# Performance work log

Hardware: AMD Instinct MI355X
Metric: run time of the kernel (lower is better)

The kernel has to match this reference:

```python
import jax, jax.numpy as jnp
import numpy as np
from jax import lax

BETA_CONTENT = 1.0   # content_addressing default beta
BETA_TOPK = 10.0     # top_k_attention default beta
GAMMA = 1.5          # location sharpening
ERASE = 0.5          # erase_strength for write
EPS = 1e-8
NEG = -1.0e9

N_SLOTS, SLOT_D, BATCH, K = 65536, 256, 512, 64


def _l2norm(x):
    # F.normalize: x / max(||x||, 1e-12)
    n = jnp.sqrt(jnp.sum(x * x, axis=-1, keepdims=True))
    return x / jnp.maximum(n, 1e-12)


def setup_inputs() -> dict:
    key = jax.random.key(0)
    k1, k2, k3, k4, k5 = jax.random.split(key, 5)
    return {
        "memory": jax.random.normal(k1, (N_SLOTS, SLOT_D), dtype=jnp.float32) * 0.1,
        "query": jax.random.normal(k2, (BATCH, SLOT_D), dtype=jnp.float32),
        "value": jax.random.normal(k3, (BATCH, SLOT_D), dtype=jnp.float32),
        "prev_weights": jax.random.uniform(k4, (BATCH, N_SLOTS), dtype=jnp.float32),
        "shift_weights": jax.random.uniform(k5, (3,), dtype=jnp.float32),
        "k": K,
    }


def reference(memory, query, value, prev_weights, shift_weights, k):
    B, N = query.shape[0], memory.shape[0]
    # --- content addressing: cosine sim + softmax ---
    qn = _l2norm(query)                      # [B,D]
    mn = _l2norm(memory)                     # [N,D]
    sim = qn @ mn.T                          # [B,N]
    w_content = jax.nn.softmax(BETA_CONTENT * sim, axis=-1)
    read_content = w_content @ memory        # [B,D] read via content weights

    # --- top-k attention: soft threshold mask + softmax ---
    kk = min(int(k), N)
    topk_vals, _ = lax.top_k(sim, kk)        # [B,kk]
    thr = topk_vals[:, -1:]                  # kth largest similarity
    mask = jax.nn.sigmoid(BETA_TOPK * (sim - thr))
    w_topk = jax.nn.softmax(BETA_TOPK * sim + (1.0 - mask) * NEG, axis=-1)
    read_topk = w_topk @ memory              # [B,D]

    # --- location addressing: conv1d shift (padding=1) + gamma sharpen ---
    p = jnp.pad(prev_weights, ((0, 0), (1, 1)))  # [B,N+2]
    shifted = (p[:, :-2] * shift_weights[0]
               + p[:, 1:-1] * shift_weights[1]
               + p[:, 2:] * shift_weights[2])     # [B,N]
    sharp = shifted ** GAMMA
    w_loc = sharp / (jnp.sum(sharp, axis=-1, keepdims=True) + EPS)

    # --- write: softmax(address), multiplicative erase, additive write ---
    w_write = jax.nn.softmax(w_loc, axis=-1)          # write() softmaxes its input
    erase_factor = jnp.prod(1.0 - w_write * ERASE, axis=0)   # [N] sequential erases fused
    new_mem = memory * erase_factor[:, None] + w_write.T @ value  # [N,D]

    return jnp.concatenate([read_content.reshape(-1),
                            read_topk.reshape(-1),
                            new_mem.reshape(-1)])
```

## Files before the change

kernel.cpp:

```cpp
#include <hip/hip_runtime.h>
#include <math.h>

#define BATCH   512
#define NSLOTS  65536
#define DIM     256

#define RB      64
#define NROWG   (BATCH/RB)
#define NCG     64
#define CPG     (NSLOTS/NCG)
#define ST      32
#define NTILES  (CPG/ST)
#define DELTA   0.009f

#define WS_QN   0
#define WS_RN   (WS_QN + BATCH*DIM)
#define WS_WST  (WS_RN + NSLOTS)
#define WS_DEN  (WS_WST + BATCH*4)
#define WS_ZS   (WS_DEN + BATCH)
#define WS_ZZ   (WS_ZS + BATCH)
#define WS_SST  (WS_ZZ + BATCH)
#define WS_VT   (WS_SST + BATCH*NCG*16*4)
#define WS_MN   (WS_VT + (BATCH*DIM)/2)
#define WS_MT   (WS_MN + ((size_t)NSLOTS*DIM)/2)

typedef __attribute__((ext_vector_type(8))) short bf16x8;
typedef __attribute__((ext_vector_type(4))) float f32x4;

__device__ inline unsigned short f2b(float x){
  unsigned u = __float_as_uint(x);
  unsigned r = u + 0x7FFFu + ((u >> 16) & 1u);
  return (unsigned short)(r >> 16);
}
__device__ inline float b2f(unsigned short b){
  return __uint_as_float(((unsigned)b) << 16);
}

__device__ __forceinline__ void gl16(const void* g, void* l){
  __builtin_amdgcn_global_load_lds(
      (__attribute__((address_space(1))) void*)g,
      (__attribute__((address_space(3))) void*)l, 16, 0, 0);
}

#define SBAR_LGKM() do{ asm volatile("s_waitcnt lgkmcnt(0)" ::: "memory"); \
                        __builtin_amdgcn_s_barrier();                      \
                        asm volatile("" ::: "memory"); }while(0)
#define SBAR_ALL()  do{ asm volatile("s_waitcnt vmcnt(0) lgkmcnt(0)" ::: "memory"); \
                        __builtin_amdgcn_s_barrier();                               \
                        asm volatile("" ::: "memory"); }while(0)

__global__ __launch_bounds__(256) void k_qnorm(const float* __restrict__ q, float* __restrict__ qn){
  int b = blockIdx.x, t = threadIdx.x;
  float v = q[b*DIM + t];
  __shared__ float red[256];
  red[t] = v*v;
  __syncthreads();
  for (int s = 128; s > 0; s >>= 1){
    if (t < s) red[t] += red[t+s];
    __syncthreads();
  }
  float n = fmaxf(sqrtf(red[0]), 1e-12f);
  qn[b*DIM + t] = v / n;
}

__global__ __launch_bounds__(256) void k_mnprep(const float* __restrict__ mem,
                                                float* __restrict__ rn,
                                                unsigned short* __restrict__ MN){
  __shared__ float rns[64];
  int t = threadIdx.x;
  int s0 = blockIdx.x * 64;
  int w = t >> 6, ln = t & 63;
  #pragma unroll
  for (int it = 0; it < 16; ++it){
    int r = it*4 + w;
    float4 v = ((const float4*)(mem + (size_t)(s0 + r)*DIM))[ln];
    float s = v.x*v.x + v.y*v.y + v.z*v.z + v.w*v.w;
    #pragma unroll
    for (int off = 32; off > 0; off >>= 1) s += __shfl_xor(s, off, 64);
    if (ln == 0){
      float inv = 1.0f / fmaxf(sqrtf(s), 1e-12f);
      rns[r] = inv; rn[s0 + r] = inv;
    }
  }
  __syncthreads();
  #pragma unroll
  for (int j = 0; j < 8; ++j){
    int id = j*256 + t;
    int r = id >> 5;
    int c = id & 31;
    float inv = rns[r];
    const float4* p = (const float4*)(mem + (size_t)(s0 + r)*DIM + c*8);
    float4 a = p[0], b = p[1];
    bf16x8 o;
    o[0]=(short)f2b(a.x*inv); o[1]=(short)f2b(a.y*inv); o[2]=(short)f2b(a.z*inv); o[3]=(short)f2b(a.w*inv);
    o[4]=(short)f2b(b.x*inv); o[5]=(short)f2b(b.y*inv); o[6]=(short)f2b(b.z*inv); o[7]=(short)f2b(b.w*inv);
    *(bf16x8*)&MN[(size_t)(s0 + r)*DIM + ((c ^ (r & 7))*8)] = o;
  }
}

__global__ __launch_bounds__(256) void k_mtprep(const float* __restrict__ mem, unsigned short* __restrict__ MT){
  __shared__ __align__(16) unsigned short tile[64][68];
  int sb = (blockIdx.x >> 2)*64, dd = (blockIdx.x & 3)*64;
  int t = threadIdx.x;
  int w = t >> 6, ln = t & 63;
  #pragma unroll
  for (int k = 0; k < 4; ++k){
    int sl = w*16 + k*4 + (ln >> 4);
    int doff = (ln & 15)*4;
    float4 f = *(const float4*)&mem[(size_t)(sb + sl)*DIM + dd + doff];
    tile[doff+0][sl] = f2b(f.x);
    tile[doff+1][sl] = f2b(f.y);
    tile[doff+2][sl] = f2b(f.z);
    tile[doff+3][sl] = f2b(f.w);
  }
  __syncthreads();
  #pragma unroll
  for (int k = 0; k < 4; ++k){
    int dl = w*16 + k*4 + (ln >> 4);
    int boff = (ln & 15)*4;
    int B = boff >> 5;
    int p = (boff >> 3) & 3;
    int pp = p ^ ((dl >> 1) & 3);
    int off = B*32 + pp*8 + (boff & 7);
    *(short4*)&MT[(size_t)(dd + dl)*NSLOTS + sb + off] = *(const short4*)&tile[dl][boff];
  }
}

__global__ __launch_bounds__(256) void k_prep(const float* __restrict__ val, unsigned short* __restrict__ VT){
  __shared__ __align__(16) unsigned short tile[64][68];
  int bb = (blockIdx.x >> 2)*64, dd = (blockIdx.x & 3)*64;
  int t = threadIdx.x;
  int w = t >> 6, ln = t & 63;
  #pragma unroll
  for (int k = 0; k < 4; ++k){
    int bl = w*16 + k*4 + (ln >> 4);
    int doff = (ln & 15)*4;
    float4 f = *(const float4*)&val[(size_t)(bb + bl)*DIM + dd + doff];
    tile[doff+0][bl] = f2b(f.x);
    tile[doff+1][bl] = f2b(f.y);
    tile[doff+2][bl] = f2b(f.z);
    tile[doff+3][bl] = f2b(f.w);
  }
  __syncthreads();
  #pragma unroll
  for (int k = 0; k < 4; ++k){
    int dl = w*16 + k*4 + (ln >> 4);
    int boff = (ln & 15)*4;
    int c  = (bb + boff) >> 5;
    int p  = (boff >> 3) & 3;
    int pp = p ^ ((dl >> 1) & 3);
    size_t addr = (size_t)c*8192 + (size_t)(dd + dl)*32 + pp*8 + (boff & 7);
    *(short4*)&VT[addr] = *(const short4*)&tile[dl][boff];
  }
}

__global__ __launch_bounds__(256) void k_ws1(const float* __restrict__ prev, const float* __restrict__ sw,
                                             float* __restrict__ zs){
  int blk = blockIdx.x;
  int b = blk >> 4, ch = blk & 15;
  int t = threadIdx.x;
  int w = t >> 6, lane = t & 63;
  float s0 = sw[0], s1 = sw[1], s2 = sw[2];
  const float* p = prev + (size_t)b*NSLOTS;
  const float4* p4 = (const float4*)p;
  float lsum = 0.f;
  #pragma unroll
  for (int k = 0; k < 4; ++k){
    int i4 = ch*1024 + k*256 + t;
    float4 f = p4[i4];
    float lft = (i4 > 0) ? p[4*i4 - 1] : 0.f;
    float rgt = (i4 < NSLOTS/4 - 1) ? p[4*i4 + 4] : 0.f;
    float sh0 = s0*lft + s1*f.x + s2*f.y;
    float sh1 = s0*f.x + s1*f.y + s2*f.z;
    float sh2 = s0*f.y + s1*f.z + s2*f.w;
    float sh3 = s0*f.z + s1*f.w + s2*rgt;
    lsum += sh0*sqrtf(sh0) + sh1*sqrtf(sh1) + sh2*sqrtf(sh2) + sh3*sqrtf(sh3);
  }
  #pragma unroll
  for (int off = 32; off > 0; off >>= 1) lsum += __shfl_xor(lsum, off, 64);
  __shared__ float wsum[4];
  if (lane == 0) wsum[w] = lsum;
  __syncthreads();
  if (t == 0) atomicAdd(&zs[b], wsum[0] + wsum[1] + wsum[2] + wsum[3]);
}

__global__ __launch_bounds__(256) void k_ws2(const float* __restrict__ prev, const float* __restrict__ sw,
                                             const float* __restrict__ zs, float* __restrict__ zz){
  int blk = blockIdx.x;
  int b = blk >> 4, ch = blk & 15;
  int t = threadIdx.x;
  int w = t >> 6, lane = t & 63;
  float s0 = sw[0], s1 = sw[1], s2 = sw[2];
  float inv_d = 1.0f / (zs[b] + 1e-8f);
  const float* p = prev + (size_t)b*NSLOTS;
  const float4* p4 = (const float4*)p;
  float lz = 0.f;
  #pragma unroll
  for (int k = 0; k < 4; ++k){
    int i4 = ch*1024 + k*256 + t;
    float4 f = p4[i4];
    float lft = (i4 > 0) ? p[4*i4 - 1] : 0.f;
    float rgt = (i4 < NSLOTS/4 - 1) ? p[4*i4 + 4] : 0.f;
    float sh0 = s0*lft + s1*f.x + s2*f.y;
    float sh1 = s0*f.x + s1*f.y + s2*f.z;
    float sh2 = s0*f.y + s1*f.z + s2*f.w;
    float sh3 = s0*f.z + s1*f.w + s2*rgt;
    lz += __expf(sh0*sqrtf(sh0)*inv_d) + __expf(sh1*sqrtf(sh1)*inv_d)
        + __expf(sh2*sqrtf(sh2)*inv_d) + __expf(sh3*sqrtf(sh3)*inv_d);
  }
  #pragma unroll
  for (int off = 32; off > 0; off >>= 1) lz += __shfl_xor(lz, off, 64);
  __shared__ float wsum[4];
  if (lane == 0) wsum[w] = lz;
  __syncthreads();
  if (t == 0) atomicAdd(&zz[b], wsum[0] + wsum[1] + wsum[2] + wsum[3]);
}

__global__ __launch_bounds__(256) void k_invd(const float* __restrict__ zs, const float* __restrict__ zz,
                                              float* __restrict__ wst){
  int b = blockIdx.x*256 + threadIdx.x;
  float4 o;
  o.x = 1.0f / (zs[b] + 1e-8f);
  o.y = 1.0f / zz[b];
  o.z = 0.f; o.w = 0.f;
  ((float4*)wst)[b] = o;
}

__global__ __launch_bounds__(256) void k_wft(const float* __restrict__ prev, const float* __restrict__ sw,
                                             const float* __restrict__ wst, unsigned short* __restrict__ WFT){
  __shared__ __align__(16) unsigned short T[64][72];
  int bs = ((int)blockIdx.x & 7) * 64;
  int ss = ((int)blockIdx.x >> 3) * 64;
  int t = threadIdx.x;
  float s0 = sw[0], s1 = sw[1], s2 = sw[2];
  int rr = t >> 4;
  int cc = t & 15;
  #pragma unroll
  for (int pass = 0; pass < 4; ++pass){
    int bl = pass*16 + rr;
    int b = bs + bl;
    const float* p = prev + (size_t)b*NSLOTS + ss;
    float2 st = *(const float2*)&wst[b*4];
    int s = cc*4;
    float4 f = *(const float4*)(p + s);
    int gs = ss + s;
    float lft = (gs > 0) ? p[s-1] : 0.f;
    float rgt = (gs + 4 < NSLOTS) ? p[s+4] : 0.f;
    float sh0 = s0*lft + s1*f.x + s2*f.y;
    float sh1 = s0*f.x + s1*f.y + s2*f.z;
    float sh2 = s0*f.y + s1*f.z + s2*f.w;
    float sh3 = s0*f.z + s1*f.w + s2*rgt;
    T[s+0][bl] = f2b(__expf(sh0*sqrtf(sh0)*st.x)*st.y);
    T[s+1][bl] = f2b(__expf(sh1*sqrtf(sh1)*st.x)*st.y);
    T[s+2][bl] = f2b(__expf(sh2*sqrtf(sh2)*st.x)*st.y);
    T[s+3][bl] = f2b(__expf(sh3*sqrtf(sh3)*st.x)*st.y);
  }
  __syncthreads();
  int sr = t >> 3;
  int ch = t & 7;
  #pragma unroll
  for (int k = 0; k < 2; ++k){
    int row = k*32 + sr;
    int c  = (bs >> 5) + (ch >> 2);
    int pp = (ch & 3) ^ ((row >> 1) & 3);
    size_t addr = (size_t)(ss >> 6)*32768 + (size_t)c*2048 + (size_t)row*32 + pp*8;
    *(bf16x8*)&WFT[addr] = *(const bf16x8*)&T[row][ch*8];
  }
}

__global__ __launch_bounds__(256, 2) void k_simfused(
    const float* __restrict__ qn,
    const unsigned short* __restrict__ MN,
    const unsigned short* __restrict__ MT,
    float* __restrict__ outc, float* __restrict__ denom, float* __restrict__ sst)
{
  __shared__ __align__(16) unsigned short Ms[2][32*256];
  __shared__ __align__(16) unsigned short Md[2][256*32];
  __shared__ __align__(16) unsigned short Plds[64*40];

  int cg = blockIdx.x, rg = blockIdx.y;
  int t = threadIdx.x;
  int w = t >> 6;
  int lane = t & 63;
  int l = lane & 15;
  int q = lane >> 4;
  int row0 = rg * RB;

  bf16x8 qa[8];
  {
    int qrow = row0 + 16*w + l;
    #pragma unroll
    for (int kk = 0; kk < 8; ++kk){
      const float4* qp = (const float4*)&qn[(size_t)qrow*DIM + 32*kk + 8*q];
      float4 a0 = qp[0], a1 = qp[1];
      bf16x8 v;
      v[0]=(short)f2b(a0.x); v[1]=(short)f2b(a0.y); v[2]=(short)f2b(a0.z); v[3]=(short)f2b(a0.w);
      v[4]=(short)f2b(a1.x); v[5]=(short)f2b(a1.y); v[6]=(short)f2b(a1.z); v[7]=(short)f2b(a1.w);
      qa[kk] = v;
    }
  }

  const char* msP = (const char*)MN + (size_t)cg*CPG*512 + (size_t)w*4096 + (size_t)lane*16;
  const char* mtP = (const char*)MT + (size_t)(w*64 + (lane>>2))*((size_t)NSLOTS*2)
                                    + (size_t)cg*CPG*2 + (size_t)(lane&3)*16;

  auto STAGE = [&](int tl, int buf){
    size_t mso = (size_t)tl*16384;
    size_t mto = (size_t)tl*64;
    #pragma unroll
    for (int j = 0; j < 4; ++j)
      gl16(msP + mso + (size_t)j*1024, &Ms[buf][w*2048 + j*512]);
    #pragma unroll
    for (int j = 0; j < 4; ++j)
      gl16(mtP + mto + (size_t)j*2097152, &Md[buf][w*2048 + j*512]);
  };

  f32x4 accO[16];
  #pragma unroll
  for (int c = 0; c < 16; ++c) accO[c] = (f32x4){0.f,0.f,0.f,0.f};

  float dsum[4] = {0.f,0.f,0.f,0.f};
  float tv0[4] = {-1e30f,-1e30f,-1e30f,-1e30f}, tv1[4] = {-1e30f,-1e30f,-1e30f,-1e30f};
  int   ti0[4] = {0,0,0,0}, ti1[4] = {0,0,0,0};

  STAGE(0, 0);
  SBAR_ALL();

  int r7 = l & 7;
  int sw2 = (q ^ ((l >> 1) & 3)) * 8;

  for (int tile = 0; tile < NTILES; ++tile){
    int cur = tile & 1;
    if (tile + 1 < NTILES) STAGE(tile + 1, cur ^ 1);
    int i0 = cg*CPG + tile*ST;

    const unsigned short* msb = &Ms[cur][0];
    f32x4 S0 = (f32x4){0.f,0.f,0.f,0.f}, S1 = (f32x4){0.f,0.f,0.f,0.f};
    #pragma unroll
    for (int kk = 0; kk < 8; ++kk){
      int c0 = ((4*kk + q) ^ r7) * 8;
      bf16x8 b0 = *(const bf16x8*)&msb[(l     )*256 + c0];
      bf16x8 b1 = *(const bf16x8*)&msb[(16 + l)*256 + c0];
      S0 = __builtin_amdgcn_mfma_f32_16x16x32_bf16(qa[kk], b0, S0, 0, 0, 0);
      S1 = __builtin_amdgcn_mfma_f32_16x16x32_bf16(qa[kk], b1, S1, 0, 0, 0);
    }

    #pragma unroll
    for (int c = 0; c < 2; ++c){
      int slot = i0 + 16*c + l;
      #pragma unroll
      for (int reg = 0; reg < 4; ++reg){
        float v = (c == 0) ? S0[reg] : S1[reg];
        bool g0 = v > tv0[reg];
        bool g1 = v > tv1[reg];
        float ov0 = tv0[reg]; int oi0 = ti0[reg];
        tv1[reg] = g0 ? ov0 : (g1 ? v : tv1[reg]);
        ti1[reg] = g0 ? oi0 : (g1 ? slot : ti1[reg]);
        tv0[reg] = g0 ? v : tv0[reg];
        ti0[reg] = g0 ? slot : ti0[reg];
        unsigned short wb = f2b(__expf(v));
        dsum[reg] += b2f(wb);
        Plds[(16*w + 4*q + reg)*40 + 16*c + l] = (short)wb;
      }
    }
    SBAR_LGKM();

    bf16x8 pa = *(const bf16x8*)&Plds[(16*w + l)*40 + 8*q];
    const unsigned short* mdb = &Md[cur][0];
    #pragma unroll
    for (int ct = 0; ct < 16; ++ct){
      bf16x8 b = *(const bf16x8*)&mdb[(16*ct + l)*32 + sw2];
      accO[ct] = __builtin_amdgcn_mfma_f32_16x16x32_bf16(pa, b, accO[ct], 0, 0, 0);
    }
    SBAR_ALL();
  }

  #pragma unroll
  for (int reg = 0; reg < 4; ++reg){
    float s = dsum[reg];
    s += __shfl_xor(s, 1, 64); s += __shfl_xor(s, 2, 64);
    s += __shfl_xor(s, 4, 64); s += __shfl_xor(s, 8, 64);
    if (l == 0) atomicAdd(&denom[row0 + 16*w + 4*q + reg], s);
  }
  #pragma unroll
  for (int reg = 0; reg < 4; ++reg){
    int row = row0 + 16*w + 4*q + reg;
    size_t base = (((size_t)row*NCG + cg)*16 + l)*2;
    float2* S2 = (float2*)sst;
    S2[base + 0] = make_float2(tv0[reg], __int_as_float(ti0[reg]));
    S2[base + 1] = make_float2(tv1[reg], __int_as_float(ti1[reg]));
  }
  #pragma unroll
  for (int ct = 0; ct < 16; ++ct){
    #pragma unroll
    for (int reg = 0; reg < 4; ++reg){
      int row = row0 + 16*w + 4*q + reg;
      atomicAdd(&outc[(size_t)row*DIM + 16*ct + l], accO[ct][reg]);
    }
  }
}

__global__ __launch_bounds__(256) void k_finish(const float* __restrict__ sst, const float* __restrict__ denom,
                                                const float* __restrict__ qn, const float* __restrict__ rn,
                                                const float* __restrict__ mem,
                                                float* __restrict__ outc, float* __restrict__ outk){
  int row = blockIdx.x, t = threadIdx.x;
  __shared__ float red[256];
  __shared__ int cnt;
  __shared__ int cidx[128];
  __shared__ float csim[128];
  __shared__ int bestIdx;
  const float2* S = (const float2*)sst + (size_t)row*NCG*16*2;
  float2 e[8];
  float lmax = -1e30f;
  #pragma unroll
  for (int k = 0; k < 8; ++k){ e[k] = S[t*8 + k]; lmax = fmaxf(lmax, e[k].x); }
  red[t] = lmax;
  __syncthreads();
  for (int s = 128; s > 0; s >>= 1){
    if (t < s) red[t] = fmaxf(red[t], red[t+s]);
    __syncthreads();
  }
  float M = red[0];
  if (t == 0) cnt = 0;
  __syncthreads();
  #pragma unroll
  for (int k = 0; k < 8; ++k){
    if (e[k].x >= M - DELTA){
      int p = atomicAdd(&cnt, 1);
      if (p < 128) cidx[p] = __float_as_int(e[k].y);
    }
  }
  __syncthreads();
  int n = min(cnt, 128);
  int wv = t >> 6, ln = t & 63;
  for (int ci = wv; ci < n; ci += 4){
    int slot = cidx[ci];
    float4 a = ((const float4*)&qn[(size_t)row*DIM])[ln];
    float4 b = ((const float4*)&mem[(size_t)slot*DIM])[ln];
    float s = a.x*b.x + a.y*b.y + a.z*b.z + a.w*b.w;
    #pragma unroll
    for (int off = 32; off > 0; off >>= 1) s += __shfl_xor(s, off, 64);
    if (ln == 0) csim[ci] = s * rn[slot];
  }
  __syncthreads();
  if (t == 0){
    float bv = -1e30f; int bi = 0x7fffffff;
    for (int i = 0; i < n; ++i){
      float v = csim[i]; int id = cidx[i];
      if (v > bv || (v == bv && id < bi)){ bv = v; bi = id; }
    }
    bestIdx = bi;
  }
  __syncthreads();
  float inv = 1.0f / denom[row];
  outc[(size_t)row*DIM + t] *= inv;
  outk[(size_t)row*DIM + t] = mem[(size_t)bestIdx*DIM + t];
}

__global__ __launch_bounds__(256, 4) void k_newmem(const float* __restrict__ mem,
                                                const unsigned short* __restrict__ VT2,
                                                const unsigned short* __restrict__ WFT2,
                                                float* __restrict__ outm){
  __shared__ __align__(16) unsigned short VB[2][256*32];
  __shared__ __align__(16) unsigned short WB[2][64*32];

  int t = threadIdx.x;
  int i0 = blockIdx.x * 64;
  int w = t >> 6;
  int lane = t & 63;
  int l = lane & 15, q = lane >> 4;

  const char* vbase = (const char*)VT2 + (size_t)w*4096 + (size_t)lane*16;
  const char* wbase = (const char*)WFT2 + (size_t)blockIdx.x*65536 + (size_t)w*1024 + (size_t)lane*16;

  auto STAGE = [&](int c, int buf){
    #pragma unroll
    for (int j = 0; j < 4; ++j)
      gl16(vbase + (size_t)c*16384 + (size_t)j*1024, &VB[buf][w*2048 + j*512]);
    gl16(wbase + (size_t)c*4096, &WB[buf][w*512]);
  };

  f32x4 accO[16];
  #pragma unroll
  for (int c = 0; c < 16; ++c) accO[c] = (f32x4){0.f,0.f,0.f,0.f};
  float epl = 1.0f;

  STAGE(0, 0);
  SBAR_ALL();

  int sw2 = (q ^ ((l >> 1) & 3)) * 8;

  #pragma unroll 1
  for (int c = 0; c < 16; ++c){
    int cur = c & 1;
    if (c + 1 < 16) STAGE(c + 1, cur ^ 1);
    bf16x8 af = *(const bf16x8*)&WB[cur][(16*w + l)*32 + sw2];
    #pragma unroll
    for (int j = 0; j < 8; ++j)
      epl *= (1.0f - 0.5f*b2f((unsigned short)af[j]));
    #pragma unroll
    for (int ct = 0; ct < 16; ++ct){
      bf16x8 bfg = *(const bf16x8*)&VB[cur][(16*ct + l)*32 + sw2];
      accO[ct] = __builtin_amdgcn_mfma_f32_16x16x32_bf16(af, bfg, accO[ct], 0, 0, 0);
    }
    SBAR_ALL();
  }

  epl *= __shfl_xor(epl, 16, 64);
  epl *= __shfl_xor(epl, 32, 64);

  #pragma unroll
  for (int reg = 0; reg < 4; ++reg){
    int so = i0 + 16*w + 4*q + reg;
    float e = __shfl(epl, 4*q + reg, 64);
    #pragma unroll
    for (int ct = 0; ct < 16; ++ct){
      int d = 16*ct + l;
      outm[(size_t)so*DIM + d] = mem[(size_t)so*DIM + d]*e + accO[ct][reg];
    }
  }
}

extern "C" void kernel_launch(void* const* d_in, const int* in_sizes, int n_in,
                              void* d_out, int out_size, void* d_ws, size_t ws_size,
                              hipStream_t stream){
  const float* mem  = (const float*)d_in[0];
  const float* qry  = (const float*)d_in[1];
  const float* val  = (const float*)d_in[2];
  const float* prev = (const float*)d_in[3];
  const float* sw   = (const float*)d_in[4];
  float* out = (float*)d_out;
  float* ws  = (float*)d_ws;

  float* qn   = ws + WS_QN;
  float* rn   = ws + WS_RN;
  float* wst  = ws + WS_WST;
  float* den  = ws + WS_DEN;
  float* zs   = ws + WS_ZS;
  float* zz   = ws + WS_ZZ;
  float* sst  = ws + WS_SST;
  unsigned short* VT = (unsigned short*)(ws + WS_VT);
  unsigned short* MN = (unsigned short*)(ws + WS_MN);
  unsigned short* MT = (unsigned short*)(ws + WS_MT);
  unsigned short* WFT = MN;

  float* out_content = out;
  float* out_topk    = out + BATCH*DIM;
  float* out_newmem  = out + 2*BATCH*DIM;

  hipMemsetAsync(out_content, 0, BATCH*DIM*sizeof(float), stream);
  hipMemsetAsync(den, 0, BATCH*sizeof(float), stream);
  hipMemsetAsync(zs, 0, 2*BATCH*sizeof(float), stream);
  hipLaunchKernelGGL(k_qnorm,   dim3(BATCH),       dim3(DIM), 0, stream, qry, qn);
  hipLaunchKernelGGL(k_mnprep,  dim3(NSLOTS/64),   dim3(256), 0, stream, mem, rn, MN);
  hipLaunchKernelGGL(k_mtprep,  dim3((NSLOTS/64)*4), dim3(256), 0, stream, mem, MT);
  hipLaunchKernelGGL(k_prep,    dim3(32),          dim3(256), 0, stream, val, VT);
  hipLaunchKernelGGL(k_ws1,     dim3(BATCH*16),    dim3(256), 0, stream, prev, sw, zs);
  hipLaunchKernelGGL(k_ws2,     dim3(BATCH*16),    dim3(256), 0, stream, prev, sw, zs, zz);
  hipLaunchKernelGGL(k_invd,    dim3(BATCH/256),   dim3(256), 0, stream, zs, zz, wst);
  hipLaunchKernelGGL(k_simfused,dim3(NCG, NROWG),  dim3(256), 0, stream, qn, MN, MT, out_content, den, sst);
  hipLaunchKernelGGL(k_wft,     dim3((NSLOTS/64)*(BATCH/64)), dim3(256), 0, stream, prev, sw, wst, WFT);
  hipLaunchKernelGGL(k_finish,  dim3(BATCH),       dim3(256), 0, stream, sst, den, qn, rn, mem, out_content, out_topk);
  hipLaunchKernelGGL(k_newmem,  dim3(NSLOTS/64),   dim3(256), 0, stream, mem, VT, WFT, out_newmem);
}
```

Baseline: 495.1 us.

## Double row tile per block and triple-buffer memory staging with one barrier

The fused similarity/softmax/read kernel now handles 128 query rows per block instead of 64, so each wave computes two 16-row groups against every staged memory tile. This halves how often the memory tiles are streamed from global memory. Staging moves from double to triple buffering with a partial vmcnt wait and a single barrier per tile, in place of two. The cost is more registers (two accumulator sets of 16 f32x4 each), more LDS, occupancy dropping to one block per CU, and half as many blocks in the grid.

```diff
diff --git a/kernel.cpp b/kernel.cpp
--- a/kernel.cpp
+++ b/kernel.cpp
@@ -5,7 +5,7 @@
 #define NSLOTS  65536
 #define DIM     256
 
-#define RB      64
+#define RB      128
 #define NROWG   (BATCH/RB)
 #define NCG     64
 #define CPG     (NSLOTS/NCG)
@@ -47,6 +47,12 @@
                         asm volatile("" ::: "memory"); }while(0)
 #define SBAR_ALL()  do{ asm volatile("s_waitcnt vmcnt(0) lgkmcnt(0)" ::: "memory"); \
                         __builtin_amdgcn_s_barrier();                               \
+                        asm volatile("" ::: "memory"); }while(0)
+#define SBAR_VM8()  do{ asm volatile("s_waitcnt vmcnt(8)" ::: "memory"); \
+                        __builtin_amdgcn_s_barrier();                     \
+                        asm volatile("" ::: "memory"); }while(0)
+#define SBAR_VM0()  do{ asm volatile("s_waitcnt vmcnt(0)" ::: "memory"); \
+                        __builtin_amdgcn_s_barrier();                     \
                         asm volatile("" ::: "memory"); }while(0)
 
 __global__ __launch_bounds__(256) void k_qnorm(const float* __restrict__ q, float* __restrict__ qn){
@@ -268,27 +274,28 @@
   }
 }
 
-__global__ __launch_bounds__(256, 2) void k_simfused(
+__global__ __launch_bounds__(256, 1) void k_simfused(
     const float* __restrict__ qn,
     const unsigned short* __restrict__ MN,
     const unsigned short* __restrict__ MT,
     float* __restrict__ outc, float* __restrict__ denom, float* __restrict__ sst)
 {
-  __shared__ __align__(16) unsigned short Ms[2][32*256];
-  __shared__ __align__(16) unsigned short Md[2][256*32];
-  __shared__ __align__(16) unsigned short Plds[64*40];
-
-  int cg = blockIdx.x, rg = blockIdx.y;
+  __shared__ __align__(16) unsigned short Ms[3][32*256];
+  __shared__ __align__(16) unsigned short Md[3][256*32];
+  __shared__ __align__(16) unsigned short Plds[128*40];
+
+  int cg = blockIdx.x, rgB = blockIdx.y;
   int t = threadIdx.x;
   int w = t >> 6;
   int lane = t & 63;
   int l = lane & 15;
   int q = lane >> 4;
-  int row0 = rg * RB;
-
-  bf16x8 qa[8];
-  {
-    int qrow = row0 + 16*w + l;
+  int row0 = rgB * RB;
+
+  bf16x8 qa[2][8];
+  #pragma unroll
+  for (int rg = 0; rg < 2; ++rg){
+    int qrow = row0 + 32*w + 16*rg + l;
     #pragma unroll
     for (int kk = 0; kk < 8; ++kk){
       const float4* qp = (const float4*)&qn[(size_t)qrow*DIM + 32*kk + 8*q];
@@ -296,7 +303,7 @@
       bf16x8 v;
       v[0]=(short)f2b(a0.x); v[1]=(short)f2b(a0.y); v[2]=(short)f2b(a0.z); v[3]=(short)f2b(a0.w);
       v[4]=(short)f2b(a1.x); v[5]=(short)f2b(a1.y); v[6]=(short)f2b(a1.z); v[7]=(short)f2b(a1.w);
-      qa[kk] = v;
+      qa[rg][kk] = v;
     }
   }
 
@@ -315,87 +322,114 @@
       gl16(mtP + mto + (size_t)j*2097152, &Md[buf][w*2048 + j*512]);
   };
 
-  f32x4 accO[16];
-  #pragma unroll
-  for (int c = 0; c < 16; ++c) accO[c] = (f32x4){0.f,0.f,0.f,0.f};
-
-  float dsum[4] = {0.f,0.f,0.f,0.f};
-  float tv0[4] = {-1e30f,-1e30f,-1e30f,-1e30f}, tv1[4] = {-1e30f,-1e30f,-1e30f,-1e30f};
-  int   ti0[4] = {0,0,0,0}, ti1[4] = {0,0,0,0};
+  f32x4 accO[2][16];
+  #pragma unroll
+  for (int rg = 0; rg < 2; ++rg)
+    #pragma unroll
+    for (int c = 0; c < 16; ++c) accO[rg][c] = (f32x4){0.f,0.f,0.f,0.f};
+
+  float dsum[2][4];
+  float tv0[2][4], tv1[2][4];
+  int   ti0[2][4], ti1[2][4];
+  #pragma unroll
+  for (int rg = 0; rg < 2; ++rg)
+    #pragma unroll
+    for (int r = 0; r < 4; ++r){
+      dsum[rg][r] = 0.f;
+      tv0[rg][r] = -1e30f; tv1[rg][r] = -1e30f;
+      ti0[rg][r] = 0; ti1[rg][r] = 0;
+    }
 
   STAGE(0, 0);
-  SBAR_ALL();
+  STAGE(1, 1);
 
   int r7 = l & 7;
   int sw2 = (q ^ ((l >> 1) & 3)) * 8;
 
   for (int tile = 0; tile < NTILES; ++tile){
-    int cur = tile & 1;
-    if (tile + 1 < NTILES) STAGE(tile + 1, cur ^ 1);
+    if (tile < NTILES-1) { SBAR_VM8(); } else { SBAR_VM0(); }
+    int cur = tile % 3;
+    if (tile + 2 < NTILES) STAGE(tile + 2, (tile + 2) % 3);
     int i0 = cg*CPG + tile*ST;
 
     const unsigned short* msb = &Ms[cur][0];
-    f32x4 S0 = (f32x4){0.f,0.f,0.f,0.f}, S1 = (f32x4){0.f,0.f,0.f,0.f};
+    f32x4 S[2][2];
+    S[0][0]=(f32x4){0.f,0.f,0.f,0.f}; S[0][1]=(f32x4){0.f,0.f,0.f,0.f};
+    S[1][0]=(f32x4){0.f,0.f,0.f,0.f}; S[1][1]=(f32x4){0.f,0.f,0.f,0.f};
     #pragma unroll
     for (int kk = 0; kk < 8; ++kk){
       int c0 = ((4*kk + q) ^ r7) * 8;
       bf16x8 b0 = *(const bf16x8*)&msb[(l     )*256 + c0];
       bf16x8 b1 = *(const bf16x8*)&msb[(16 + l)*256 + c0];
-      S0 = __builtin_amdgcn_mfma_f32_16x16x32_bf16(qa[kk], b0, S0, 0, 0, 0);
-      S1 = __builtin_amdgcn_mfma_f32_16x16x32_bf16(qa[kk], b1, S1, 0, 0, 0);
-    }
-
-    #pragma unroll
-    for (int c = 0; c < 2; ++c){
-      int slot = i0 + 16*c + l;
+      S[0][0] = __builtin_amdgcn_mfma_f32_16x16x32_bf16(qa[0][kk], b0, S[0][0], 0, 0, 0);
+      S[0][1] = __builtin_amdgcn_mfma_f32_16x16x32_bf16(qa[0][kk], b1, S[0][1], 0, 0, 0);
+      S[1][0] = __builtin_amdgcn_mfma_f32_16x16x32_bf16(qa[1][kk], b0, S[1][0], 0, 0, 0);
+      S[1][1] = __builtin_amdgcn_mfma_f32_16x16x32_bf16(qa[1][kk], b1, S[1][1], 0, 0, 0);
+    }
+
+    #pragma unroll
+    for (int rg = 0; rg < 2; ++rg){
+      #pragma unroll
+      for (int c = 0; c < 2; ++c){
+        int slot = i0 + 16*c + l;
+        #pragma unroll
+        for (int reg = 0; reg < 4; ++reg){
+          float v = S[rg][c][reg];
+          bool g0 = v > tv0[rg][reg];
+          bool g1 = v > tv1[rg][reg];
+          float ov0 = tv0[rg][reg]; int oi0 = ti0[rg][reg];
+          tv1[rg][reg] = g0 ? ov0 : (g1 ? v : tv1[rg][reg]);
+          ti1[rg][reg] = g0 ? oi0 : (g1 ? slot : ti1[rg][reg]);
+          tv0[rg][reg] = g0 ? v : tv0[rg][reg];
+          ti0[rg][reg] = g0 ? slot : ti0[rg][reg];
+          unsigned short wb = f2b(__expf(v));
+          dsum[rg][reg] += b2f(wb);
+          Plds[(32*w + 16*rg + 4*q + reg)*40 + 16*c + l] = (short)wb;
+        }
+      }
+    }
+
+    bf16x8 pa0 = *(const bf16x8*)&Plds[(32*w + l)*40 + 8*q];
+    bf16x8 pa1 = *(const bf16x8*)&Plds[(32*w + 16 + l)*40 + 8*q];
+    const unsigned short* mdb = &Md[cur][0];
+    #pragma unroll
+    for (int ct = 0; ct < 16; ++ct){
+      bf16x8 b = *(const bf16x8*)&mdb[(16*ct + l)*32 + sw2];
+      accO[0][ct] = __builtin_amdgcn_mfma_f32_16x16x32_bf16(pa0, b, accO[0][ct], 0, 0, 0);
+      accO[1][ct] = __builtin_amdgcn_mfma_f32_16x16x32_bf16(pa1, b, accO[1][ct], 0, 0, 0);
+    }
+  }
+
+  #pragma unroll
+  for (int rg = 0; rg < 2; ++rg){
+    #pragma unroll
+    for (int reg = 0; reg < 4; ++reg){
+      float s = dsum[rg][reg];
+      s += __shfl_xor(s, 1, 64); s += __shfl_xor(s, 2, 64);
+      s += __shfl_xor(s, 4, 64); s += __shfl_xor(s, 8, 64);
+      if (l == 0) atomicAdd(&denom[row0 + 32*w + 16*rg + 4*q + reg], s);
+    }
+  }
+  #pragma unroll
+  for (int rg = 0; rg < 2; ++rg){
+    #pragma unroll
+    for (int reg = 0; reg < 4; ++reg){
+      int row = row0 + 32*w + 16*rg + 4*q + reg;
+      size_t base = (((size_t)row*NCG + cg)*16 + l)*2;
+      float2* S2 = (float2*)sst;
+      S2[base + 0] = make_float2(tv0[rg][reg], __int_as_float(ti0[rg][reg]));
+      S2[base + 1] = make_float2(tv1[rg][reg], __int_as_float(ti1[rg][reg]));
+    }
+  }
+  #pragma unroll
+  for (int rg = 0; rg < 2; ++rg){
+    #pragma unroll
+    for (int ct = 0; ct < 16; ++ct){
       #pragma unroll
       for (int reg = 0; reg < 4; ++reg){
-        float v = (c == 0) ? S0[reg] : S1[reg];
-        bool g0 = v > tv0[reg];
-        bool g1 = v > tv1[reg];
-        float ov0 = tv0[reg]; int oi0 = ti0[reg];
-        tv1[reg] = g0 ? ov0 : (g1 ? v : tv1[reg]);
-        ti1[reg] = g0 ? oi0 : (g1 ? slot : ti1[reg]);
-        tv0[reg] = g0 ? v : tv0[reg];
-        ti0[reg] = g0 ? slot : ti0[reg];
-        unsigned short wb = f2b(__expf(v));
-        dsum[reg] += b2f(wb);
-        Plds[(16*w + 4*q + reg)*40 + 16*c + l] = (short)wb;
+        int row = row0 + 32*w + 16*rg + 4*q + reg;
+        atomicAdd(&outc[(size_t)row*DIM + 16*ct + l], accO[rg][ct][reg]);
       }
-    }
-    SBAR_LGKM();
-
-    bf16x8 pa = *(const bf16x8*)&Plds[(16*w + l)*40 + 8*q];
-    const unsigned short* mdb = &Md[cur][0];
-    #pragma unroll
-    for (int ct = 0; ct < 16; ++ct){
-      bf16x8 b = *(const bf16x8*)&mdb[(16*ct + l)*32 + sw2];
-      accO[ct] = __builtin_amdgcn_mfma_f32_16x16x32_bf16(pa, b, accO[ct], 0, 0, 0);
-    }
-    SBAR_ALL();
-  }
-
-  #pragma unroll
-  for (int reg = 0; reg < 4; ++reg){
-    float s = dsum[reg];
-    s += __shfl_xor(s, 1, 64); s += __shfl_xor(s, 2, 64);
-    s += __shfl_xor(s, 4, 64); s += __shfl_xor(s, 8, 64);
-    if (l == 0) atomicAdd(&denom[row0 + 16*w + 4*q + reg], s);
-  }
-  #pragma unroll
-  for (int reg = 0; reg < 4; ++reg){
-    int row = row0 + 16*w + 4*q + reg;
-    size_t base = (((size_t)row*NCG + cg)*16 + l)*2;
-    float2* S2 = (float2*)sst;
-    S2[base + 0] = make_float2(tv0[reg], __int_as_float(ti0[reg]));
-    S2[base + 1] = make_float2(tv1[reg], __int_as_float(ti1[reg]));
-  }
-  #pragma unroll
-  for (int ct = 0; ct < 16; ++ct){
-    #pragma unroll
-    for (int reg = 0; reg < 4; ++reg){
-      int row = row0 + 16*w + 4*q + reg;
-      atomicAdd(&outc[(size_t)row*DIM + 16*ct + l], accO[ct][reg]);
     }
   }
 }
```

Result: slower. 515.2 us (+4.1%).
